# Optimization experiments

Measured on AMD Instinct MI355X. Metric: run time of the kernel, lower is better.

Reference implementation:

```python
import jax, jax.numpy as jnp
import numpy as np

K = 3
STRIDE = 1
PAD = 1
DIL = 1


def conv2d(x, w, b, stride, pad, dil):
    y = jax.lax.conv_general_dilated(
        x, w, (stride, stride), [(pad, pad), (pad, pad)],
        rhs_dilation=(dil, dil), dimension_numbers=("NCHW", "OIHW", "NCHW"))
    return y + b[None, :, None, None]


def bilinear_gather(img, ys, xs):
    # img: (C,H,W); ys,xs: (KK,Ho,Wo) pixel coords.
    # grid_sample(mode=bilinear, padding_mode=zeros, align_corners=True):
    # out-of-range corners contribute 0, interpolation weights unchanged.
    H, W = img.shape[-2:]
    y0 = jnp.floor(ys)
    x0 = jnp.floor(xs)
    wy1 = ys - y0
    wx1 = xs - x0
    wy0 = 1.0 - wy1
    wx0 = 1.0 - wx1

    def g(yc, xc):
        yi = yc.astype(jnp.int32)
        xi = xc.astype(jnp.int32)
        valid = (yi >= 0) & (yi < H) & (xi >= 0) & (xi < W)
        yi = jnp.clip(yi, 0, H - 1)
        xi = jnp.clip(xi, 0, W - 1)
        v = img[:, yi, xi]  # (C,KK,Ho,Wo)
        return v * valid[None].astype(img.dtype)

    return (g(y0, x0) * (wy0 * wx0)[None]
            + g(y0, x0 + 1.0) * (wy0 * wx1)[None]
            + g(y0 + 1.0, x0) * (wy1 * wx0)[None]
            + g(y0 + 1.0, x0 + 1.0) * (wy1 * wx1)[None])


def setup_inputs() -> dict:
    key = jax.random.key(0)
    ks = jax.random.split(key, 4)
    B, C_in, H, W = 8, 64, 96, 96
    C_out = 64
    x = jax.random.normal(ks[0], (B, C_in, H, W), dtype=jnp.float32)
    weight = jax.random.normal(ks[1], (C_out, C_in, K, K), dtype=jnp.float32) * 0.05
    bias = jax.random.normal(ks[2], (C_out,), dtype=jnp.float32) * 0.01
    off_w = jax.random.normal(ks[3], (2 * K * K, C_in, K, K), dtype=jnp.float32) * 0.05
    off_b = jnp.zeros((2 * K * K,), dtype=jnp.float32)
    return {"x": x, "weight": weight, "bias": bias, "off_w": off_w, "off_b": off_b}


def reference(x, weight, bias, off_w, off_b):
    B, C, H, W = x.shape
    Ho = (H + 2 * PAD - DIL * (K - 1) - 1) // STRIDE + 1
    Wo = (W + 2 * PAD - DIL * (K - 1) - 1) // STRIDE + 1

    offsets = conv2d(x, off_w, off_b, STRIDE, PAD, DIL)  # (B,2*K*K,Ho,Wo)
    off = offsets.reshape(B, K * K, 2, Ho, Wo)

    # Base sampling grid (note: original code does NOT subtract padding; kept faithful).
    by, bx = jnp.meshgrid(jnp.arange(Ho, dtype=x.dtype), jnp.arange(Wo, dtype=x.dtype), indexing="ij")
    by = by * STRIDE + (K // 2) * DIL
    bx = bx * STRIDE + (K // 2) * DIL
    ko = jnp.arange(-(K // 2), K // 2 + 1, dtype=x.dtype)
    ky, kx = jnp.meshgrid(ko, ko, indexing="ij")

    sy = by[None, None] + ky.reshape(1, -1, 1, 1) + off[:, :, 0]  # (B,KK,Ho,Wo)
    sx = bx[None, None] + kx.reshape(1, -1, 1, 1) + off[:, :, 1]

    sampled = jax.vmap(bilinear_gather)(x, sy, sx)  # (B,C,KK,Ho,Wo)

    wflat = weight.reshape(weight.shape[0], C, K * K)  # (O,C,KK)
    out = jnp.einsum("bckhw,ock->bohw", sampled, wflat)
    return out + bias[None, :, None, None]
```

## Files before the change

### kernel.cpp

```cpp
#include <hip/hip_runtime.h>

#define HH 96
#define WW 96
#define HW 9216
#define CIN 64
#define COUT 64
#define NB 8

typedef __bf16 bf16x8 __attribute__((ext_vector_type(8)));
typedef float  f32x4  __attribute__((ext_vector_type(4)));

__device__ __forceinline__ unsigned short f2bf_bits(float f) {
    unsigned u = __float_as_uint(f);
    unsigned r = u + 0x7FFFu + ((u >> 16) & 1u);
    return (unsigned short)(r >> 16);
}
__device__ __forceinline__ float bf2f(unsigned short s) {
    return __uint_as_float(((unsigned)s) << 16);
}

__global__ __launch_bounds__(256) void xcvt_prep(const float* __restrict__ x,
                                                 const float* __restrict__ weight,
                                                 const float* __restrict__ off_w,
                                                 unsigned short* __restrict__ xt,
                                                 unsigned short* __restrict__ wTb,
                                                 unsigned short* __restrict__ owTb) {
    int bid   = blockIdx.x;
    int t     = threadIdx.x;
    int b     = bid & 7;
    int pbase = (bid >> 3) * 64;
    int pl    = t & 63;
    int q     = t >> 6;
    int p     = pbase + pl;

    const float* xp = x + ((size_t)(b * 64 + q * 16)) * HW + p;
    unsigned short hbits[16];
#pragma unroll
    for (int i = 0; i < 16; ++i) hbits[i] = f2bf_bits(xp[(size_t)i * HW]);

    uint4 w0, w1;
    w0.x = hbits[0]  | (hbits[1]  << 16);
    w0.y = hbits[2]  | (hbits[3]  << 16);
    w0.z = hbits[4]  | (hbits[5]  << 16);
    w0.w = hbits[6]  | (hbits[7]  << 16);
    w1.x = hbits[8]  | (hbits[9]  << 16);
    w1.y = hbits[10] | (hbits[11] << 16);
    w1.z = hbits[12] | (hbits[13] << 16);
    w1.w = hbits[14] | (hbits[15] << 16);
    unsigned short* dst = xt + ((size_t)(b * HW + p)) * 64 + q * 16;
    *(uint4*)dst       = w0;
    *(uint4*)(dst + 8) = w1;

    if (bid < 216) {
        int i = bid * 256 + t;
        if (i < 36864) {
            int tap = i >> 12;
            int co  = (i >> 6) & 63;
            int c   = i & 63;
            wTb[i] = f2bf_bits(weight[(co * 64 + c) * 9 + tap]);
        } else {
            int f  = i - 36864;
            int j  = f / 576;
            int kk = f - j * 576;
            int tap = kk >> 6;
            int c   = kk & 63;
            owTb[f] = (j < 18) ? f2bf_bits(off_w[((j * 64 + c) * 9) + tap]) : (unsigned short)0;
        }
    }
}

__global__ __launch_bounds__(256, 4) void offs_mfma(const unsigned short* __restrict__ xt,
                                                    const unsigned short* __restrict__ owTb,
                                                    const float* __restrict__ ob,
                                                    float* __restrict__ off) {
    __shared__ unsigned short S[64 * 72];

    int bid   = blockIdx.x;
    int t     = threadIdx.x;
    int b     = bid & 7;
    int pbase = (bid >> 3) * 64;

    int pl = t & 63;
    int cg = t >> 6;
    int px = pbase + pl;
    int h  = px / WW;
    int w  = px - h * WW;

    int ln = t & 15;
    int qd = (t >> 4) & 3;
    int pt = t >> 6;

    f32x4 accj[2] = {{0.f, 0.f, 0.f, 0.f}, {0.f, 0.f, 0.f, 0.f}};

    const unsigned short* xb = xt + (size_t)b * HW * 64;

    for (int tap = 0; tap < 9; ++tap) {
        int r  = tap / 3, s = tap - r * 3;
        int iy = h - 1 + r, ix = w - 1 + s;
        bool valid = (iy >= 0) & (iy < HH) & (ix >= 0) & (ix < WW);
        uint4 va = {0u, 0u, 0u, 0u}, vb = {0u, 0u, 0u, 0u};
        if (valid) {
            const uint4* p = (const uint4*)(xb + ((size_t)(iy * WW + ix)) * 64 + cg * 16);
            va = p[0];
            vb = p[1];
        }
        *(uint4*)&S[pl * 72 + cg * 16]     = va;
        *(uint4*)&S[pl * 72 + cg * 16 + 8] = vb;
        __syncthreads();

        bf16x8 a0 = *(const bf16x8*)&S[(pt * 16 + ln) * 72 + qd * 8];
        bf16x8 a1 = *(const bf16x8*)&S[(pt * 16 + ln) * 72 + 32 + qd * 8];
#pragma unroll
        for (int jt = 0; jt < 2; ++jt) {
            const unsigned short* brow = owTb + (size_t)(jt * 16 + ln) * 576 + tap * 64 + qd * 8;
            bf16x8 b0 = *(const bf16x8*)brow;
            bf16x8 b1 = *(const bf16x8*)(brow + 32);
            accj[jt] = __builtin_amdgcn_mfma_f32_16x16x32_bf16(a0, b0, accj[jt], 0, 0, 0);
            accj[jt] = __builtin_amdgcn_mfma_f32_16x16x32_bf16(a1, b1, accj[jt], 0, 0, 0);
        }
        __syncthreads();
    }

    int pxo = pbase + pt * 16 + qd * 4;
    {
        float bv = ob[ln];
        float4 st;
        st.x = accj[0].x + bv; st.y = accj[0].y + bv;
        st.z = accj[0].z + bv; st.w = accj[0].w + bv;
        *(float4*)(off + ((size_t)(b * 18 + ln)) * HW + pxo) = st;
    }
    if (ln < 2) {
        int   j  = 16 + ln;
        float bv = ob[j];
        float4 st;
        st.x = accj[1].x + bv; st.y = accj[1].y + bv;
        st.z = accj[1].z + bv; st.w = accj[1].w + bv;
        *(float4*)(off + ((size_t)(b * 18 + j)) * HW + pxo) = st;
    }
}

__global__ __launch_bounds__(256, 4) void deform_main(const unsigned short* __restrict__ xt,
                                                      const unsigned short* __restrict__ wTb,
                                                      const float* __restrict__ bias,
                                                      const float* __restrict__ off,
                                                      float* __restrict__ out) {
    __shared__ unsigned short S[64 * 72];
    __shared__ unsigned short Wk[64 * 72];

    int bid   = blockIdx.x;
    int t     = threadIdx.x;
    int b     = bid & 7;
    int pbase = (bid >> 3) * 64;

    int pl = t & 63;
    int cg = t >> 6;
    int px = pbase + pl;
    int h  = px / WW;
    int w  = px - h * WW;

    int ln = t & 15;
    int qd = (t >> 4) & 3;
    int ct = t >> 6;

    const unsigned short* xb = xt + (size_t)b * HW * 64;
    const float* offb = off + (size_t)b * 18 * HW + px;

    float offy[9], offx[9];
#pragma unroll
    for (int k = 0; k < 9; ++k) {
        offy[k] = offb[(2 * k) * HW];
        offx[k] = offb[(2 * k + 1) * HW];
    }

    f32x4 acc[4] = {{0.f,0.f,0.f,0.f},{0.f,0.f,0.f,0.f},{0.f,0.f,0.f,0.f},{0.f,0.f,0.f,0.f}};

    for (int tap = 0; tap < 9; ++tap) {
        int   r = tap / 3, s = tap - r * 3;
        float sy = (float)(h + r) + offy[tap];
        float sx = (float)(w + s) + offx[tap];
        float fy = floorf(sy), fx = floorf(sx);
        int   y0 = (int)fy, x0 = (int)fx;
        int   y1 = y0 + 1, x1 = x0 + 1;
        float wy1 = sy - fy, wx1 = sx - fx;
        float wy0 = 1.f - wy1, wx0 = 1.f - wx1;

        float m00 = (y0 >= 0 && y0 < HH && x0 >= 0 && x0 < WW) ? 1.f : 0.f;
        float m01 = (y0 >= 0 && y0 < HH && x1 >= 0 && x1 < WW) ? 1.f : 0.f;
        float m10 = (y1 >= 0 && y1 < HH && x0 >= 0 && x0 < WW) ? 1.f : 0.f;
        float m11 = (y1 >= 0 && y1 < HH && x1 >= 0 && x1 < WW) ? 1.f : 0.f;

        int cy0 = min(max(y0, 0), HH - 1), cy1 = min(max(y1, 0), HH - 1);
        int cx0 = min(max(x0, 0), WW - 1), cx1 = min(max(x1, 0), WW - 1);
        float w00 = wy0 * wx0 * m00, w01 = wy0 * wx1 * m01;
        float w10 = wy1 * wx0 * m10, w11 = wy1 * wx1 * m11;

        const uint4* p00 = (const uint4*)(xb + ((size_t)(cy0 * WW + cx0)) * 64 + cg * 16);
        const uint4* p01 = (const uint4*)(xb + ((size_t)(cy0 * WW + cx1)) * 64 + cg * 16);
        const uint4* p10 = (const uint4*)(xb + ((size_t)(cy1 * WW + cx0)) * 64 + cg * 16);
        const uint4* p11 = (const uint4*)(xb + ((size_t)(cy1 * WW + cx1)) * 64 + cg * 16);
        uint4 c00[2] = {p00[0], p00[1]};
        uint4 c01[2] = {p01[0], p01[1]};
        uint4 c10[2] = {p10[0], p10[1]};
        uint4 c11[2] = {p11[0], p11[1]};

        unsigned short ov[16];
#pragma unroll
        for (int g = 0; g < 2; ++g) {
            const unsigned short* q00 = (const unsigned short*)&c00[g];
            const unsigned short* q01 = (const unsigned short*)&c01[g];
            const unsigned short* q10 = (const unsigned short*)&c10[g];
            const unsigned short* q11 = (const unsigned short*)&c11[g];
#pragma unroll
            for (int i = 0; i < 8; ++i) {
                float v = w00 * bf2f(q00[i]) + w01 * bf2f(q01[i])
                        + w10 * bf2f(q10[i]) + w11 * bf2f(q11[i]);
                ov[g * 8 + i] = f2bf_bits(v);
            }
        }
        uint4 s0, s1;
        s0.x = ov[0]  | (ov[1]  << 16); s0.y = ov[2]  | (ov[3]  << 16);
        s0.z = ov[4]  | (ov[5]  << 16); s0.w = ov[6]  | (ov[7]  << 16);
        s1.x = ov[8]  | (ov[9]  << 16); s1.y = ov[10] | (ov[11] << 16);
        s1.z = ov[12] | (ov[13] << 16); s1.w = ov[14] | (ov[15] << 16);
        *(uint4*)&S[pl * 72 + cg * 16]     = s0;
        *(uint4*)&S[pl * 72 + cg * 16 + 8] = s1;

        {
            const uint4* wsrc = (const uint4*)(wTb + (size_t)tap * 4096);
            uint4 a  = wsrc[2 * t];
            uint4 b2 = wsrc[2 * t + 1];
            int co = t >> 2, c0 = (t & 3) * 16;
            *(uint4*)&Wk[co * 72 + c0]     = a;
            *(uint4*)&Wk[co * 72 + c0 + 8] = b2;
        }
        __syncthreads();

        bf16x8 b0 = *(const bf16x8*)&Wk[(ct * 16 + ln) * 72 + qd * 8];
        bf16x8 b1 = *(const bf16x8*)&Wk[(ct * 16 + ln) * 72 + 32 + qd * 8];
#pragma unroll
        for (int pt = 0; pt < 4; ++pt) {
            bf16x8 a0 = *(const bf16x8*)&S[(pt * 16 + ln) * 72 + qd * 8];
            bf16x8 a1 = *(const bf16x8*)&S[(pt * 16 + ln) * 72 + 32 + qd * 8];
            acc[pt] = __builtin_amdgcn_mfma_f32_16x16x32_bf16(a0, b0, acc[pt], 0, 0, 0);
            acc[pt] = __builtin_amdgcn_mfma_f32_16x16x32_bf16(a1, b1, acc[pt], 0, 0, 0);
        }
        __syncthreads();
    }

    int   co = ct * 16 + ln;
    float bv = bias[co];
    float* ob2 = out + ((size_t)(b * 64 + co)) * HW + pbase + qd * 4;
#pragma unroll
    for (int pt = 0; pt < 4; ++pt) {
        float4 st;
        st.x = acc[pt].x + bv; st.y = acc[pt].y + bv;
        st.z = acc[pt].z + bv; st.w = acc[pt].w + bv;
        *(float4*)(ob2 + pt * 16) = st;
    }
}

extern "C" void kernel_launch(void* const* d_in, const int* in_sizes, int n_in,
                              void* d_out, int out_size, void* d_ws, size_t ws_size,
                              hipStream_t stream) {
    const float* x      = (const float*)d_in[0];
    const float* weight = (const float*)d_in[1];
    const float* bias   = (const float*)d_in[2];
    const float* off_w  = (const float*)d_in[3];
    const float* off_b  = (const float*)d_in[4];
    float* out = (float*)d_out;

    float*          offbuf = (float*)d_ws;
    unsigned short* xt     = (unsigned short*)(offbuf + 1327104);
    unsigned short* wTb    = xt + 4718592;
    unsigned short* owTb   = wTb + 36864;

    hipLaunchKernelGGL(xcvt_prep,   dim3(1152), dim3(256), 0, stream,
                       x, weight, off_w, xt, wTb, owTb);
    hipLaunchKernelGGL(offs_mfma,   dim3(1152), dim3(256), 0, stream,
                       xt, owTb, off_b, offbuf);
    hipLaunchKernelGGL(deform_main, dim3(1152), dim3(256), 0, stream,
                       xt, wTb, bias, offbuf, out);
}
```

Before: 161.7 us.

## Software-pipeline gather loads across taps and coalesce transposed bf16 stores

The deform and offset-conv kernels now issue the global loads for tap t+1 (bilinear corner gathers, weight tiles, B-fragments) into registers before processing tap t. This overlaps memory latency with the interpolation math and MFMA work. The prep kernel now transposes through shared memory so each block writes its NHWC bf16 tile contiguously. The launch-bounds occupancy hints are dropped, so register use will rise and occupancy may fall.

New measurement: 163.2 us. Within noise of the previous version (+0.9%).

```diff
diff --git a/kernel.cpp b/kernel.cpp
--- a/kernel.cpp
+++ b/kernel.cpp
@@ -3,12 +3,12 @@
 #define HH 96
 #define WW 96
 #define HW 9216
-#define CIN 64
-#define COUT 64
 #define NB 8
 
 typedef __bf16 bf16x8 __attribute__((ext_vector_type(8)));
 typedef float  f32x4  __attribute__((ext_vector_type(4)));
+
+union BF8 { uint4 u; bf16x8 v; unsigned short s[8]; };
 
 __device__ __forceinline__ unsigned short f2bf_bits(float f) {
     unsigned u = __float_as_uint(f);
@@ -25,31 +25,33 @@
                                                  unsigned short* __restrict__ xt,
                                                  unsigned short* __restrict__ wTb,
                                                  unsigned short* __restrict__ owTb) {
+    __shared__ unsigned short T[64 * 72];
     int bid   = blockIdx.x;
     int t     = threadIdx.x;
     int b     = bid & 7;
     int pbase = (bid >> 3) * 64;
     int pl    = t & 63;
     int q     = t >> 6;
-    int p     = pbase + pl;
-
-    const float* xp = x + ((size_t)(b * 64 + q * 16)) * HW + p;
-    unsigned short hbits[16];
-#pragma unroll
-    for (int i = 0; i < 16; ++i) hbits[i] = f2bf_bits(xp[(size_t)i * HW]);
+
+    const float* xp = x + ((size_t)(b * 64 + q * 16)) * HW + pbase + pl;
+    unsigned short hb[16];
+#pragma unroll
+    for (int i = 0; i < 16; ++i) hb[i] = f2bf_bits(xp[(size_t)i * HW]);
 
     uint4 w0, w1;
-    w0.x = hbits[0]  | (hbits[1]  << 16);
-    w0.y = hbits[2]  | (hbits[3]  << 16);
-    w0.z = hbits[4]  | (hbits[5]  << 16);
-    w0.w = hbits[6]  | (hbits[7]  << 16);
-    w1.x = hbits[8]  | (hbits[9]  << 16);
-    w1.y = hbits[10] | (hbits[11] << 16);
-    w1.z = hbits[12] | (hbits[13] << 16);
-    w1.w = hbits[14] | (hbits[15] << 16);
-    unsigned short* dst = xt + ((size_t)(b * HW + p)) * 64 + q * 16;
-    *(uint4*)dst       = w0;
-    *(uint4*)(dst + 8) = w1;
+    w0.x = hb[0]  | (hb[1]  << 16); w0.y = hb[2]  | (hb[3]  << 16);
+    w0.z = hb[4]  | (hb[5]  << 16); w0.w = hb[6]  | (hb[7]  << 16);
+    w1.x = hb[8]  | (hb[9]  << 16); w1.y = hb[10] | (hb[11] << 16);
+    w1.z = hb[12] | (hb[13] << 16); w1.w = hb[14] | (hb[15] << 16);
+    *(uint4*)&T[pl * 72 + q * 16]     = w0;
+    *(uint4*)&T[pl * 72 + q * 16 + 8] = w1;
+    __syncthreads();
+
+    uint4 a  = *(const uint4*)&T[(t >> 2) * 72 + (t & 3) * 16];
+    uint4 b2 = *(const uint4*)&T[(t >> 2) * 72 + (t & 3) * 16 + 8];
+    unsigned short* dst = xt + ((size_t)(b * HW + pbase)) * 64 + t * 16;
+    *(uint4*)dst       = a;
+    *(uint4*)(dst + 8) = b2;
 
     if (bid < 216) {
         int i = bid * 256 + t;
@@ -59,20 +61,20 @@
             int c   = i & 63;
             wTb[i] = f2bf_bits(weight[(co * 64 + c) * 9 + tap]);
         } else {
-            int f  = i - 36864;
-            int j  = f / 576;
-            int kk = f - j * 576;
+            int f   = i - 36864;
+            int j   = f / 576;
+            int kk  = f - j * 576;
             int tap = kk >> 6;
             int c   = kk & 63;
-            owTb[f] = (j < 18) ? f2bf_bits(off_w[((j * 64 + c) * 9) + tap]) : (unsigned short)0;
-        }
-    }
-}
-
-__global__ __launch_bounds__(256, 4) void offs_mfma(const unsigned short* __restrict__ xt,
-                                                    const unsigned short* __restrict__ owTb,
-                                                    const float* __restrict__ ob,
-                                                    float* __restrict__ off) {
+            owTb[f] = (j < 18) ? f2bf_bits(off_w[(j * 64 + c) * 9 + tap]) : (unsigned short)0;
+        }
+    }
+}
+
+__global__ __launch_bounds__(256) void offs_mfma(const unsigned short* __restrict__ xt,
+                                                 const unsigned short* __restrict__ owTb,
+                                                 const float* __restrict__ ob,
+                                                 float* __restrict__ off) {
     __shared__ unsigned short S[64 * 72];
 
     int bid   = blockIdx.x;
@@ -94,31 +96,54 @@
 
     const unsigned short* xb = xt + (size_t)b * HW * 64;
 
+    uint4 pa, pb, paN, pbN;
+    uint4 br00, br01, br10, br11, br00N, br01N, br10N, br11N;
+
+    {
+        int  iy = h - 1, ix = w - 1;
+        bool valid = (iy >= 0) & (ix >= 0);
+        int  cy = max(iy, 0), cx = max(ix, 0);
+        const uint4* p = (const uint4*)(xb + ((size_t)(cy * WW + cx)) * 64 + cg * 16);
+        pa = p[0]; pb = p[1];
+        if (!valid) { pa = make_uint4(0,0,0,0); pb = make_uint4(0,0,0,0); }
+        const unsigned short* b0p = owTb + (size_t)ln * 576 + qd * 8;
+        const unsigned short* b1p = owTb + (size_t)(16 + ln) * 576 + qd * 8;
+        br00 = *(const uint4*)b0p;  br01 = *(const uint4*)(b0p + 32);
+        br10 = *(const uint4*)b1p;  br11 = *(const uint4*)(b1p + 32);
+    }
+
     for (int tap = 0; tap < 9; ++tap) {
-        int r  = tap / 3, s = tap - r * 3;
-        int iy = h - 1 + r, ix = w - 1 + s;
-        bool valid = (iy >= 0) & (iy < HH) & (ix >= 0) & (ix < WW);
-        uint4 va = {0u, 0u, 0u, 0u}, vb = {0u, 0u, 0u, 0u};
-        if (valid) {
-            const uint4* p = (const uint4*)(xb + ((size_t)(iy * WW + ix)) * 64 + cg * 16);
-            va = p[0];
-            vb = p[1];
-        }
-        *(uint4*)&S[pl * 72 + cg * 16]     = va;
-        *(uint4*)&S[pl * 72 + cg * 16 + 8] = vb;
+        if (tap < 8) {
+            int  tn = tap + 1;
+            int  r  = tn / 3, s = tn - r * 3;
+            int  iy = h - 1 + r, ix = w - 1 + s;
+            bool valid = (iy >= 0) & (iy < HH) & (ix >= 0) & (ix < WW);
+            int  cy = min(max(iy, 0), HH - 1), cx = min(max(ix, 0), WW - 1);
+            const uint4* p = (const uint4*)(xb + ((size_t)(cy * WW + cx)) * 64 + cg * 16);
+            paN = p[0]; pbN = p[1];
+            if (!valid) { paN = make_uint4(0,0,0,0); pbN = make_uint4(0,0,0,0); }
+            const unsigned short* b0p = owTb + (size_t)ln * 576 + tn * 64 + qd * 8;
+            const unsigned short* b1p = owTb + (size_t)(16 + ln) * 576 + tn * 64 + qd * 8;
+            br00N = *(const uint4*)b0p;  br01N = *(const uint4*)(b0p + 32);
+            br10N = *(const uint4*)b1p;  br11N = *(const uint4*)(b1p + 32);
+        }
+
+        *(uint4*)&S[pl * 72 + cg * 16]     = pa;
+        *(uint4*)&S[pl * 72 + cg * 16 + 8] = pb;
         __syncthreads();
 
-        bf16x8 a0 = *(const bf16x8*)&S[(pt * 16 + ln) * 72 + qd * 8];
-        bf16x8 a1 = *(const bf16x8*)&S[(pt * 16 + ln) * 72 + 32 + qd * 8];
-#pragma unroll
-        for (int jt = 0; jt < 2; ++jt) {
-            const unsigned short* brow = owTb + (size_t)(jt * 16 + ln) * 576 + tap * 64 + qd * 8;
-            bf16x8 b0 = *(const bf16x8*)brow;
-            bf16x8 b1 = *(const bf16x8*)(brow + 32);
-            accj[jt] = __builtin_amdgcn_mfma_f32_16x16x32_bf16(a0, b0, accj[jt], 0, 0, 0);
-            accj[jt] = __builtin_amdgcn_mfma_f32_16x16x32_bf16(a1, b1, accj[jt], 0, 0, 0);
-        }
+        BF8 a0, a1, u00, u01, u10, u11;
+        a0.u = *(const uint4*)&S[(pt * 16 + ln) * 72 + qd * 8];
+        a1.u = *(const uint4*)&S[(pt * 16 + ln) * 72 + 32 + qd * 8];
+        u00.u = br00; u01.u = br01; u10.u = br10; u11.u = br11;
+        accj[0] = __builtin_amdgcn_mfma_f32_16x16x32_bf16(a0.v, u00.v, accj[0], 0, 0, 0);
+        accj[0] = __builtin_amdgcn_mfma_f32_16x16x32_bf16(a1.v, u01.v, accj[0], 0, 0, 0);
+        accj[1] = __builtin_amdgcn_mfma_f32_16x16x32_bf16(a0.v, u10.v, accj[1], 0, 0, 0);
+        accj[1] = __builtin_amdgcn_mfma_f32_16x16x32_bf16(a1.v, u11.v, accj[1], 0, 0, 0);
         __syncthreads();
+
+        pa = paN; pb = pbN;
+        br00 = br00N; br01 = br01N; br10 = br10N; br11 = br11N;
     }
 
     int pxo = pbase + pt * 16 + qd * 4;
@@ -139,11 +164,11 @@
     }
 }
 
-__global__ __launch_bounds__(256, 4) void deform_main(const unsigned short* __restrict__ xt,
-                                                      const unsigned short* __restrict__ wTb,
-                                                      const float* __restrict__ bias,
-                                                      const float* __restrict__ off,
-                                                      float* __restrict__ out) {
+__global__ __launch_bounds__(256) void deform_main(const unsigned short* __restrict__ xt,
+                                                   const unsigned short* __restrict__ wTb,
+                                                   const float* __restrict__ bias,
+                                                   const float* __restrict__ off,
+                                                   float* __restrict__ out) {
     __shared__ unsigned short S[64 * 72];
     __shared__ unsigned short Wk[64 * 72];
 
@@ -174,78 +199,97 @@
 
     f32x4 acc[4] = {{0.f,0.f,0.f,0.f},{0.f,0.f,0.f,0.f},{0.f,0.f,0.f,0.f},{0.f,0.f,0.f,0.f}};
 
+    uint4 c00a, c00b, c01a, c01b, c10a, c10b, c11a, c11b, wk0, wk1;
+    uint4 c00aN, c00bN, c01aN, c01bN, c10aN, c10bN, c11aN, c11bN, wk0N, wk1N;
+    float w00, w01, w10, w11, w00N, w01N, w10N, w11N;
+
+#define ISSUE_TAP(TAP, A00,B00,A01,B01,A10,B10,A11,B11, WA,WB, W0,W1,W2,W3)            \
+    {                                                                                   \
+        int   r = (TAP) / 3, s = (TAP) - r * 3;                                         \
+        float sy = (float)(h + r) + offy[(TAP)];                                        \
+        float sx = (float)(w + s) + offx[(TAP)];                                        \
+        float fy = floorf(sy), fx = floorf(sx);                                         \
+        int   y0 = (int)fy, x0 = (int)fx;                                               \
+        int   y1 = y0 + 1, x1 = x0 + 1;                                                 \
+        float wy1 = sy - fy, wx1 = sx - fx;                                             \
+        float wy0 = 1.f - wy1, wx0 = 1.f - wx1;                                         \
+        float m00 = (y0 >= 0 && y0 < HH && x0 >= 0 && x0 < WW) ? 1.f : 0.f;             \
+        float m01 = (y0 >= 0 && y0 < HH && x1 >= 0 && x1 < WW) ? 1.f : 0.f;             \
+        float m10 = (y1 >= 0 && y1 < HH && x0 >= 0 && x0 < WW) ? 1.f : 0.f;             \
+        float m11 = (y1 >= 0 && y1 < HH && x1 >= 0 && x1 < WW) ? 1.f : 0.f;             \
+        int cy0 = min(max(y0, 0), HH - 1), cy1 = min(max(y1, 0), HH - 1);               \
+        int cx0 = min(max(x0, 0), WW - 1), cx1 = min(max(x1, 0), WW - 1);               \
+        W0 = wy0 * wx0 * m00; W1 = wy0 * wx1 * m01;                                     \
+        W2 = wy1 * wx0 * m10; W3 = wy1 * wx1 * m11;                                     \
+        const uint4* p00 = (const uint4*)(xb + ((size_t)(cy0 * WW + cx0)) * 64 + cg * 16); \
+        const uint4* p01 = (const uint4*)(xb + ((size_t)(cy0 * WW + cx1)) * 64 + cg * 16); \
+        const uint4* p10 = (const uint4*)(xb + ((size_t)(cy1 * WW + cx0)) * 64 + cg * 16); \
+        const uint4* p11 = (const uint4*)(xb + ((size_t)(cy1 * WW + cx1)) * 64 + cg * 16); \
+        A00 = p00[0]; B00 = p00[1];                                                     \
+        A01 = p01[0]; B01 = p01[1];                                                     \
+        A10 = p10[0]; B10 = p10[1];                                                     \
+        A11 = p11[0]; B11 = p11[1];                                                     \
+        const uint4* wsrc = (const uint4*)(wTb + (size_t)(TAP) * 4096);                 \
+        WA = wsrc[2 * t]; WB = wsrc[2 * t + 1];                                         \
+    }
+
+    ISSUE_TAP(0, c00a,c00b,c01a,c01b,c10a,c10b,c11a,c11b, wk0,wk1, w00,w01,w10,w11);
+
     for (int tap = 0; tap < 9; ++tap) {
-        int   r = tap / 3, s = tap - r * 3;
-        float sy = (float)(h + r) + offy[tap];
-        float sx = (float)(w + s) + offx[tap];
-        float fy = floorf(sy), fx = floorf(sx);
-        int   y0 = (int)fy, x0 = (int)fx;
-        int   y1 = y0 + 1, x1 = x0 + 1;
-        float wy1 = sy - fy, wx1 = sx - fx;
-        float wy0 = 1.f - wy1, wx0 = 1.f - wx1;
-
-        float m00 = (y0 >= 0 && y0 < HH && x0 >= 0 && x0 < WW) ? 1.f : 0.f;
-        float m01 = (y0 >= 0 && y0 < HH && x1 >= 0 && x1 < WW) ? 1.f : 0.f;
-        float m10 = (y1 >= 0 && y1 < HH && x0 >= 0 && x0 < WW) ? 1.f : 0.f;
-        float m11 = (y1 >= 0 && y1 < HH && x1 >= 0 && x1 < WW) ? 1.f : 0.f;
-
-        int cy0 = min(max(y0, 0), HH - 1), cy1 = min(max(y1, 0), HH - 1);
-        int cx0 = min(max(x0, 0), WW - 1), cx1 = min(max(x1, 0), WW - 1);
-        float w00 = wy0 * wx0 * m00, w01 = wy0 * wx1 * m01;
-        float w10 = wy1 * wx0 * m10, w11 = wy1 * wx1 * m11;
-
-        const uint4* p00 = (const uint4*)(xb + ((size_t)(cy0 * WW + cx0)) * 64 + cg * 16);
-        const uint4* p01 = (const uint4*)(xb + ((size_t)(cy0 * WW + cx1)) * 64 + cg * 16);
-        const uint4* p10 = (const uint4*)(xb + ((size_t)(cy1 * WW + cx0)) * 64 + cg * 16);
-        const uint4* p11 = (const uint4*)(xb + ((size_t)(cy1 * WW + cx1)) * 64 + cg * 16);
-        uint4 c00[2] = {p00[0], p00[1]};
-        uint4 c01[2] = {p01[0], p01[1]};
-        uint4 c10[2] = {p10[0], p10[1]};
-        uint4 c11[2] = {p11[0], p11[1]};
-
-        unsigned short ov[16];
-#pragma unroll
-        for (int g = 0; g < 2; ++g) {
-            const unsigned short* q00 = (const unsigned short*)&c00[g];
-            const unsigned short* q01 = (const unsigned short*)&c01[g];
-            const unsigned short* q10 = (const unsigned short*)&c10[g];
-            const unsigned short* q11 = (const unsigned short*)&c11[g];
+        if (tap < 8) {
+            ISSUE_TAP(tap + 1, c00aN,c00bN,c01aN,c01bN,c10aN,c10bN,c11aN,c11bN,
+                      wk0N,wk1N, w00N,w01N,w10N,w11N);
+        }
+
+        {
+            BF8 q00a, q00b, q01a, q01b, q10a, q10b, q11a, q11b;
+            q00a.u = c00a; q00b.u = c00b; q01a.u = c01a; q01b.u = c01b;
+            q10a.u = c10a; q10b.u = c10b; q11a.u = c11a; q11b.u = c11b;
+            unsigned short ov[16];
 #pragma unroll
             for (int i = 0; i < 8; ++i) {
-                float v = w00 * bf2f(q00[i]) + w01 * bf2f(q01[i])
-                        + w10 * bf2f(q10[i]) + w11 * bf2f(q11[i]);
-                ov[g * 8 + i] = f2bf_bits(v);
+                float v0 = w00 * bf2f(q00a.s[i]) + w01 * bf2f(q01a.s[i])
+                         + w10 * bf2f(q10a.s[i]) + w11 * bf2f(q11a.s[i]);
+                float v1 = w00 * bf2f(q00b.s[i]) + w01 * bf2f(q01b.s[i])
+                         + w10 * bf2f(q10b.s[i]) + w11 * bf2f(q11b.s[i]);
+                ov[i]     = f2bf_bits(v0);
+                ov[8 + i] = f2bf_bits(v1);
             }
-        }
-        uint4 s0, s1;
-        s0.x = ov[0]  | (ov[1]  << 16); s0.y = ov[2]  | (ov[3]  << 16);
-        s0.z = ov[4]  | (ov[5]  << 16); s0.w = ov[6]  | (ov[7]  << 16);
-        s1.x = ov[8]  | (ov[9]  << 16); s1.y = ov[10] | (ov[11] << 16);
-        s1.z = ov[12] | (ov[13] << 16); s1.w = ov[14] | (ov[15] << 16);
-        *(uint4*)&S[pl * 72 + cg * 16]     = s0;
-        *(uint4*)&S[pl * 72 + cg * 16 + 8] = s1;
+            uint4 s0, s1;
+            s0.x = ov[0]  | (ov[1]  << 16); s0.y = ov[2]  | (ov[3]  << 16);
+            s0.z = ov[4]  | (ov[5]  << 16); s0.w = ov[6]  | (ov[7]  << 16);
+            s1.x = ov[8]  | (ov[9]  << 16); s1.y = ov[10] | (ov[11] << 16);
+            s1.z = ov[12] | (ov[13] << 16); s1.w = ov[14] | (ov[15] << 16);
+            *(uint4*)&S[pl * 72 + cg * 16]     = s0;
+            *(uint4*)&S[pl * 72 + cg * 16 + 8] = s1;
+
+            int co = t >> 2, c0 = (t & 3) * 16;
+            *(uint4*)&Wk[co * 72 + c0]     = wk0;
+            *(uint4*)&Wk[co * 72 + c0 + 8] = wk1;
+        }
+        __syncthreads();
 
         {
-            const uint4* wsrc = (const uint4*)(wTb + (size_t)tap * 4096);
-            uint4 a  = wsrc[2 * t];
-            uint4 b2 = wsrc[2 * t + 1];
-            int co = t >> 2, c0 = (t & 3) * 16;
-            *(uint4*)&Wk[co * 72 + c0]     = a;
-            *(uint4*)&Wk[co * 72 + c0 + 8] = b2;
+            BF8 b0, b1;
+            b0.u = *(const uint4*)&Wk[(ct * 16 + ln) * 72 + qd * 8];
+            b1.u = *(const uint4*)&Wk[(ct * 16 + ln) * 72 + 32 + qd * 8];
+#pragma unroll
+            for (int pt = 0; pt < 4; ++pt) {
+                BF8 a0, a1;
+                a0.u = *(const uint4*)&S[(pt * 16 + ln) * 72 + qd * 8];
+                a1.u = *(const uint4*)&S[(pt * 16 + ln) * 72 + 32 + qd * 8];
+                acc[pt] = __builtin_amdgcn_mfma_f32_16x16x32_bf16(a0.v, b0.v, acc[pt], 0, 0, 0);
+                acc[pt] = __builtin_amdgcn_mfma_f32_16x16x32_bf16(a1.v, b1.v, acc[pt], 0, 0, 0);
+            }
         }
         __syncthreads();
 
-        bf16x8 b0 = *(const bf16x8*)&Wk[(ct * 16 + ln) * 72 + qd * 8];
-        bf16x8 b1 = *(const bf16x8*)&Wk[(ct * 16 + ln) * 72 + 32 + qd * 8];
-#pragma unroll
-        for (int pt = 0; pt < 4; ++pt) {
-            bf16x8 a0 = *(const bf16x8*)&S[(pt * 16 + ln) * 72 + qd * 8];
-            bf16x8 a1 = *(const bf16x8*)&S[(pt * 16 + ln) * 72 + 32 + qd * 8];
-            acc[pt] = __builtin_amdgcn_mfma_f32_16x16x32_bf16(a0, b0, acc[pt], 0, 0, 0);
-            acc[pt] = __builtin_amdgcn_mfma_f32_16x16x32_bf16(a1, b1, acc[pt], 0, 0, 0);
-        }
-        __syncthreads();
-    }
+        c00a = c00aN; c00b = c00bN; c01a = c01aN; c01b = c01bN;
+        c10a = c10aN; c10b = c10bN; c11a = c11aN; c11b = c11bN;
+        wk0 = wk0N; wk1 = wk1N;
+        w00 = w00N; w01 = w01N; w10 = w10N; w11 = w11N;
+    }
+#undef ISSUE_TAP
 
     int   co = ct * 16 + ln;
     float bv = bias[co];
```

## Coalesce pixel-major gathers, XOR-swizzle LDS tiles, and prefetch offsets per tap

Applied to the files above, without the earlier changes.

The gather work is remapped so that 8 consecutive threads each read 16 bytes of one pixel's 64-channel row, giving coalesced 128-byte reads, and each thread handles two pixels. The LDS tiles drop the 72-element padding in favour of an XOR swizzle on 16-byte chunks to avoid bank conflicts. The transpose in xcvt_prep is staged through shared memory so its global writes become contiguous. In deform_main the offsets for the next tap are loaded during the current tap instead of all 18 values up front, and the occupancy hint in launch_bounds is removed.

Measured after the change: 136.4 us. 15.7% less time.

```diff
diff --git a/kernel.cpp b/kernel.cpp
--- a/kernel.cpp
+++ b/kernel.cpp
@@ -3,12 +3,12 @@
 #define HH 96
 #define WW 96
 #define HW 9216
-#define CIN 64
-#define COUT 64
 #define NB 8
 
 typedef __bf16 bf16x8 __attribute__((ext_vector_type(8)));
 typedef float  f32x4  __attribute__((ext_vector_type(4)));
+
+union BF8 { uint4 u; bf16x8 v; unsigned short s[8]; };
 
 __device__ __forceinline__ unsigned short f2bf_bits(float f) {
     unsigned u = __float_as_uint(f);
@@ -17,6 +17,27 @@
 }
 __device__ __forceinline__ float bf2f(unsigned short s) {
     return __uint_as_float(((unsigned)s) << 16);
+}
+
+__device__ __forceinline__ void bl_setup(int h, int w, int r, int s, float oy, float ox,
+                                         int* a, float* wg) {
+    float sy = (float)(h + r) + oy;
+    float sx = (float)(w + s) + ox;
+    float fy = floorf(sy), fx = floorf(sx);
+    int   y0 = (int)fy, x0 = (int)fx;
+    int   y1 = y0 + 1, x1 = x0 + 1;
+    float wy1 = sy - fy, wx1 = sx - fx;
+    float wy0 = 1.f - wy1, wx0 = 1.f - wx1;
+    float m00 = (y0 >= 0 && y0 < HH && x0 >= 0 && x0 < WW) ? 1.f : 0.f;
+    float m01 = (y0 >= 0 && y0 < HH && x1 >= 0 && x1 < WW) ? 1.f : 0.f;
+    float m10 = (y1 >= 0 && y1 < HH && x0 >= 0 && x0 < WW) ? 1.f : 0.f;
+    float m11 = (y1 >= 0 && y1 < HH && x1 >= 0 && x1 < WW) ? 1.f : 0.f;
+    int cy0 = min(max(y0, 0), HH - 1), cy1 = min(max(y1, 0), HH - 1);
+    int cx0 = min(max(x0, 0), WW - 1), cx1 = min(max(x1, 0), WW - 1);
+    a[0] = (cy0 * WW + cx0) * 64;  a[1] = (cy0 * WW + cx1) * 64;
+    a[2] = (cy1 * WW + cx0) * 64;  a[3] = (cy1 * WW + cx1) * 64;
+    wg[0] = wy0 * wx0 * m00;  wg[1] = wy0 * wx1 * m01;
+    wg[2] = wy1 * wx0 * m10;  wg[3] = wy1 * wx1 * m11;
 }
 
 __global__ __launch_bounds__(256) void xcvt_prep(const float* __restrict__ x,
@@ -25,31 +46,35 @@
                                                  unsigned short* __restrict__ xt,
                                                  unsigned short* __restrict__ wTb,
                                                  unsigned short* __restrict__ owTb) {
+    __shared__ unsigned short T[64 * 64];
     int bid   = blockIdx.x;
     int t     = threadIdx.x;
     int b     = bid & 7;
     int pbase = (bid >> 3) * 64;
     int pl    = t & 63;
     int q     = t >> 6;
-    int p     = pbase + pl;
-
-    const float* xp = x + ((size_t)(b * 64 + q * 16)) * HW + p;
-    unsigned short hbits[16];
-#pragma unroll
-    for (int i = 0; i < 16; ++i) hbits[i] = f2bf_bits(xp[(size_t)i * HW]);
+
+    const float* xp = x + ((size_t)(b * 64 + q * 16)) * HW + pbase + pl;
+    unsigned short hb[16];
+#pragma unroll
+    for (int i = 0; i < 16; ++i) hb[i] = f2bf_bits(xp[(size_t)i * HW]);
 
     uint4 w0, w1;
-    w0.x = hbits[0]  | (hbits[1]  << 16);
-    w0.y = hbits[2]  | (hbits[3]  << 16);
-    w0.z = hbits[4]  | (hbits[5]  << 16);
-    w0.w = hbits[6]  | (hbits[7]  << 16);
-    w1.x = hbits[8]  | (hbits[9]  << 16);
-    w1.y = hbits[10] | (hbits[11] << 16);
-    w1.z = hbits[12] | (hbits[13] << 16);
-    w1.w = hbits[14] | (hbits[15] << 16);
-    unsigned short* dst = xt + ((size_t)(b * HW + p)) * 64 + q * 16;
-    *(uint4*)dst       = w0;
-    *(uint4*)(dst + 8) = w1;
+    w0.x = hb[0]  | (hb[1]  << 16); w0.y = hb[2]  | (hb[3]  << 16);
+    w0.z = hb[4]  | (hb[5]  << 16); w0.w = hb[6]  | (hb[7]  << 16);
+    w1.x = hb[8]  | (hb[9]  << 16); w1.y = hb[10] | (hb[11] << 16);
+    w1.z = hb[12] | (hb[13] << 16); w1.w = hb[14] | (hb[15] << 16);
+    int sw = pl & 7;
+    *(uint4*)&T[pl * 64 + (((2 * q)     ^ sw) << 3)] = w0;
+    *(uint4*)&T[pl * 64 + (((2 * q + 1) ^ sw) << 3)] = w1;
+    __syncthreads();
+
+    int row = t >> 2, rs = row & 7;
+    uint4 a  = *(const uint4*)&T[row * 64 + ((((t & 3) * 2)     ^ rs) << 3)];
+    uint4 b2 = *(const uint4*)&T[row * 64 + ((((t & 3) * 2 + 1) ^ rs) << 3)];
+    unsigned short* dst = xt + ((size_t)(b * HW + pbase)) * 64 + t * 16;
+    *(uint4*)dst       = a;
+    *(uint4*)(dst + 8) = b2;
 
     if (bid < 216) {
         int i = bid * 256 + t;
@@ -59,64 +84,72 @@
             int c   = i & 63;
             wTb[i] = f2bf_bits(weight[(co * 64 + c) * 9 + tap]);
         } else {
-            int f  = i - 36864;
-            int j  = f / 576;
-            int kk = f - j * 576;
+            int f   = i - 36864;
+            int j   = f / 576;
+            int kk  = f - j * 576;
             int tap = kk >> 6;
             int c   = kk & 63;
-            owTb[f] = (j < 18) ? f2bf_bits(off_w[((j * 64 + c) * 9) + tap]) : (unsigned short)0;
-        }
-    }
-}
-
-__global__ __launch_bounds__(256, 4) void offs_mfma(const unsigned short* __restrict__ xt,
-                                                    const unsigned short* __restrict__ owTb,
-                                                    const float* __restrict__ ob,
-                                                    float* __restrict__ off) {
-    __shared__ unsigned short S[64 * 72];
+            owTb[f] = (j < 18) ? f2bf_bits(off_w[(j * 64 + c) * 9 + tap]) : (unsigned short)0;
+        }
+    }
+}
+
+__global__ __launch_bounds__(256) void offs_mfma(const unsigned short* __restrict__ xt,
+                                                 const unsigned short* __restrict__ owTb,
+                                                 const float* __restrict__ ob,
+                                                 float* __restrict__ off) {
+    __shared__ unsigned short S[64 * 64];
 
     int bid   = blockIdx.x;
     int t     = threadIdx.x;
     int b     = bid & 7;
     int pbase = (bid >> 3) * 64;
 
-    int pl = t & 63;
-    int cg = t >> 6;
-    int px = pbase + pl;
-    int h  = px / WW;
-    int w  = px - h * WW;
+    int e    = t & 7;
+    int base = t >> 3;
+    int px0  = pbase + base;
+    int px1  = px0 + 32;
+    int h0 = px0 / WW, w0 = px0 - h0 * WW;
+    int h1 = px1 / WW, w1 = px1 - h1 * WW;
+    int sw = base & 7;
 
     int ln = t & 15;
     int qd = (t >> 4) & 3;
     int pt = t >> 6;
 
     f32x4 accj[2] = {{0.f, 0.f, 0.f, 0.f}, {0.f, 0.f, 0.f, 0.f}};
-
     const unsigned short* xb = xt + (size_t)b * HW * 64;
 
     for (int tap = 0; tap < 9; ++tap) {
-        int r  = tap / 3, s = tap - r * 3;
-        int iy = h - 1 + r, ix = w - 1 + s;
-        bool valid = (iy >= 0) & (iy < HH) & (ix >= 0) & (ix < WW);
-        uint4 va = {0u, 0u, 0u, 0u}, vb = {0u, 0u, 0u, 0u};
-        if (valid) {
-            const uint4* p = (const uint4*)(xb + ((size_t)(iy * WW + ix)) * 64 + cg * 16);
-            va = p[0];
-            vb = p[1];
-        }
-        *(uint4*)&S[pl * 72 + cg * 16]     = va;
-        *(uint4*)&S[pl * 72 + cg * 16 + 8] = vb;
+        int r = tap / 3, s = tap - r * 3;
+
+        int  iy0 = h0 - 1 + r, ix0 = w0 - 1 + s;
+        bool v0  = (iy0 >= 0) & (iy0 < HH) & (ix0 >= 0) & (ix0 < WW);
+        int  a0  = (min(max(iy0, 0), HH - 1) * WW + min(max(ix0, 0), WW - 1)) * 64;
+        int  iy1 = h1 - 1 + r, ix1 = w1 - 1 + s;
+        bool v1  = (iy1 >= 0) & (iy1 < HH) & (ix1 >= 0) & (ix1 < WW);
+        int  a1  = (min(max(iy1, 0), HH - 1) * WW + min(max(ix1, 0), WW - 1)) * 64;
+
+        uint4 p0 = *(const uint4*)(xb + a0 + e * 8);
+        uint4 p1 = *(const uint4*)(xb + a1 + e * 8);
+        if (!v0) p0 = make_uint4(0, 0, 0, 0);
+        if (!v1) p1 = make_uint4(0, 0, 0, 0);
+        *(uint4*)&S[base * 64 + ((e ^ sw) << 3)]        = p0;
+        *(uint4*)&S[(base + 32) * 64 + ((e ^ sw) << 3)] = p1;
         __syncthreads();
 
-        bf16x8 a0 = *(const bf16x8*)&S[(pt * 16 + ln) * 72 + qd * 8];
-        bf16x8 a1 = *(const bf16x8*)&S[(pt * 16 + ln) * 72 + 32 + qd * 8];
+        int  row = pt * 16 + ln, rs = row & 7;
+        BF8  fa0, fa1;
+        fa0.u = *(const uint4*)&S[row * 64 + ((qd       ^ rs) << 3)];
+        fa1.u = *(const uint4*)&S[row * 64 + (((qd + 4) ^ rs) << 3)];
 #pragma unroll
         for (int jt = 0; jt < 2; ++jt) {
             const unsigned short* brow = owTb + (size_t)(jt * 16 + ln) * 576 + tap * 64 + qd * 8;
-            bf16x8 b0 = *(const bf16x8*)brow;
-            bf16x8 b1 = *(const bf16x8*)(brow + 32);
-            accj[jt] = __builtin_amdgcn_mfma_f32_16x16x32_bf16(a0, b0, accj[jt], 0, 0, 0);
-            accj[jt] = __builtin_amdgcn_mfma_f32_16x16x32_bf16(a1, b1, accj[jt], 0, 0, 0);
+            BF8 fb0, fb1;
+            fb0.u = *(const uint4*)brow;
+            fb1.u = *(const uint4*)(brow + 32);
+            accj[jt] = __builtin_amdgcn_mfma_f32_16x16x32_bf16(fa0.v, fb0.v, accj[jt], 0, 0, 0);
+            accj[jt] = __builtin_amdgcn_mfma_f32_16x16x32_bf16(fa1.v, fb1.v, accj[jt], 0, 0, 0);
         }
         __syncthreads();
     }
@@ -139,112 +172,119 @@
     }
 }
 
-__global__ __launch_bounds__(256, 4) void deform_main(const unsigned short* __restrict__ xt,
-                                                      const unsigned short* __restrict__ wTb,
-                                                      const float* __restrict__ bias,
-                                                      const float* __restrict__ off,
-                                                      float* __restrict__ out) {
-    __shared__ unsigned short S[64 * 72];
-    __shared__ unsigned short Wk[64 * 72];
+__global__ __launch_bounds__(256) void deform_main(const unsigned short* __restrict__ xt,
+                                                   const unsigned short* __restrict__ wTb,
+                                                   const float* __restrict__ bias,
+                                                   const float* __restrict__ off,
+                                                   float* __restrict__ out) {
+    __shared__ unsigned short S[64 * 64];
+    __shared__ unsigned short Wk[64 * 64];
 
     int bid   = blockIdx.x;
     int t     = threadIdx.x;
     int b     = bid & 7;
     int pbase = (bid >> 3) * 64;
 
-    int pl = t & 63;
-    int cg = t >> 6;
-    int px = pbase + pl;
-    int h  = px / WW;
-    int w  = px - h * WW;
+    int e    = t & 7;
+    int base = t >> 3;
+    int px0  = pbase + base;
+    int px1  = px0 + 32;
+    int h0 = px0 / WW, w0 = px0 - h0 * WW;
+    int h1 = px1 / WW, w1 = px1 - h1 * WW;
+    int sw = base & 7;
 
     int ln = t & 15;
     int qd = (t >> 4) & 3;
     int ct = t >> 6;
 
     const unsigned short* xb = xt + (size_t)b * HW * 64;
-    const float* offb = off + (size_t)b * 18 * HW + px;
-
-    float offy[9], offx[9];
-#pragma unroll
-    for (int k = 0; k < 9; ++k) {
-        offy[k] = offb[(2 * k) * HW];
-        offx[k] = offb[(2 * k + 1) * HW];
-    }
+    const float* offb = off + (size_t)b * 18 * HW;
 
     f32x4 acc[4] = {{0.f,0.f,0.f,0.f},{0.f,0.f,0.f,0.f},{0.f,0.f,0.f,0.f},{0.f,0.f,0.f,0.f}};
 
+    float oy0 = offb[0 * HW + px0], ox0 = offb[1 * HW + px0];
+    float oy1 = offb[0 * HW + px1], ox1 = offb[1 * HW + px1];
+
     for (int tap = 0; tap < 9; ++tap) {
-        int   r = tap / 3, s = tap - r * 3;
-        float sy = (float)(h + r) + offy[tap];
-        float sx = (float)(w + s) + offx[tap];
-        float fy = floorf(sy), fx = floorf(sx);
-        int   y0 = (int)fy, x0 = (int)fx;
-        int   y1 = y0 + 1, x1 = x0 + 1;
-        float wy1 = sy - fy, wx1 = sx - fx;
-        float wy0 = 1.f - wy1, wx0 = 1.f - wx1;
-
-        float m00 = (y0 >= 0 && y0 < HH && x0 >= 0 && x0 < WW) ? 1.f : 0.f;
-        float m01 = (y0 >= 0 && y0 < HH && x1 >= 0 && x1 < WW) ? 1.f : 0.f;
-        float m10 = (y1 >= 0 && y1 < HH && x0 >= 0 && x0 < WW) ? 1.f : 0.f;
-        float m11 = (y1 >= 0 && y1 < HH && x1 >= 0 && x1 < WW) ? 1.f : 0.f;
-
-        int cy0 = min(max(y0, 0), HH - 1), cy1 = min(max(y1, 0), HH - 1);
-        int cx0 = min(max(x0, 0), WW - 1), cx1 = min(max(x1, 0), WW - 1);
-        float w00 = wy0 * wx0 * m00, w01 = wy0 * wx1 * m01;
-        float w10 = wy1 * wx0 * m10, w11 = wy1 * wx1 * m11;
-
-        const uint4* p00 = (const uint4*)(xb + ((size_t)(cy0 * WW + cx0)) * 64 + cg * 16);
-        const uint4* p01 = (const uint4*)(xb + ((size_t)(cy0 * WW + cx1)) * 64 + cg * 16);
-        const uint4* p10 = (const uint4*)(xb + ((size_t)(cy1 * WW + cx0)) * 64 + cg * 16);
-        const uint4* p11 = (const uint4*)(xb + ((size_t)(cy1 * WW + cx1)) * 64 + cg * 16);
-        uint4 c00[2] = {p00[0], p00[1]};
-        uint4 c01[2] = {p01[0], p01[1]};
-        uint4 c10[2] = {p10[0], p10[1]};
-        uint4 c11[2] = {p11[0], p11[1]};
-
-        unsigned short ov[16];
-#pragma unroll
-        for (int g = 0; g < 2; ++g) {
-            const unsigned short* q00 = (const unsigned short*)&c00[g];
-            const unsigned short* q01 = (const unsigned short*)&c01[g];
-            const unsigned short* q10 = (const unsigned short*)&c10[g];
-            const unsigned short* q11 = (const unsigned short*)&c11[g];
-#pragma unroll
-            for (int i = 0; i < 8; ++i) {
-                float v = w00 * bf2f(q00[i]) + w01 * bf2f(q01[i])
-                        + w10 * bf2f(q10[i]) + w11 * bf2f(q11[i]);
-                ov[g * 8 + i] = f2bf_bits(v);
-            }
-        }
-        uint4 s0, s1;
-        s0.x = ov[0]  | (ov[1]  << 16); s0.y = ov[2]  | (ov[3]  << 16);
-        s0.z = ov[4]  | (ov[5]  << 16); s0.w = ov[6]  | (ov[7]  << 16);
-        s1.x = ov[8]  | (ov[9]  << 16); s1.y = ov[10] | (ov[11] << 16);
-        s1.z = ov[12] | (ov[13] << 16); s1.w = ov[14] | (ov[15] << 16);
-        *(uint4*)&S[pl * 72 + cg * 16]     = s0;
-        *(uint4*)&S[pl * 72 + cg * 16 + 8] = s1;
+        int r = tap / 3, s = tap - r * 3;
+
+        int   a0[4], a1[4];
+        float g0[4], g1[4];
+        bl_setup(h0, w0, r, s, oy0, ox0, a0, g0);
+        bl_setup(h1, w1, r, s, oy1, ox1, a1, g1);
+
+        uint4 cA[4], cB[4];
+#pragma unroll
+        for (int c = 0; c < 4; ++c) cA[c] = *(const uint4*)(xb + a0[c] + e * 8);
+#pragma unroll
+        for (int c = 0; c < 4; ++c) cB[c] = *(const uint4*)(xb + a1[c] + e * 8);
+
+        float oy0N = 0.f, ox0N = 0.f, oy1N = 0.f, ox1N = 0.f;
+        if (tap < 8) {
+            oy0N = offb[(2 * tap + 2) * HW + px0]; ox0N = offb[(2 * tap + 3) * HW + px0];
+            oy1N = offb[(2 * tap + 2) * HW + px1]; ox1N = offb[(2 * tap + 3) * HW + px1];
+        }
 
         {
             const uint4* wsrc = (const uint4*)(wTb + (size_t)tap * 4096);
-            uint4 a  = wsrc[2 * t];
-            uint4 b2 = wsrc[2 * t + 1];
-            int co = t >> 2, c0 = (t & 3) * 16;
-            *(uint4*)&Wk[co * 72 + c0]     = a;
-            *(uint4*)&Wk[co * 72 + c0 + 8] = b2;
+            uint4 wa = wsrc[2 * t];
+            uint4 wb = wsrc[2 * t + 1];
+            int co = t >> 2, cs = co & 7;
+            int c0 = (t & 3) * 2;
+            *(uint4*)&Wk[co * 64 + ((c0       ^ cs) << 3)] = wa;
+            *(uint4*)&Wk[co * 64 + (((c0 + 1) ^ cs) << 3)] = wb;
+        }
+
+        {
+            BF8 q0, q1, q2, q3;
+            q0.u = cA[0]; q1.u = cA[1]; q2.u = cA[2]; q3.u = cA[3];
+            unsigned short ov[8];
+#pragma unroll
+            for (int i = 0; i < 8; ++i) {
+                float v = g0[0] * bf2f(q0.s[i]) + g0[1] * bf2f(q1.s[i])
+                        + g0[2] * bf2f(q2.s[i]) + g0[3] * bf2f(q3.s[i]);
+                ov[i] = f2bf_bits(v);
+            }
+            uint4 sv;
+            sv.x = ov[0] | (ov[1] << 16); sv.y = ov[2] | (ov[3] << 16);
+            sv.z = ov[4] | (ov[5] << 16); sv.w = ov[6] | (ov[7] << 16);
+            *(uint4*)&S[base * 64 + ((e ^ sw) << 3)] = sv;
+        }
+        {
+            BF8 q0, q1, q2, q3;
+            q0.u = cB[0]; q1.u = cB[1]; q2.u = cB[2]; q3.u = cB[3];
+            unsigned short ov[8];
+#pragma unroll
+            for (int i = 0; i < 8; ++i) {
+                float v = g1[0] * bf2f(q0.s[i]) + g1[1] * bf2f(q1.s[i])
+                        + g1[2] * bf2f(q2.s[i]) + g1[3] * bf2f(q3.s[i]);
+                ov[i] = f2bf_bits(v);
+            }
+            uint4 sv;
+            sv.x = ov[0] | (ov[1] << 16); sv.y = ov[2] | (ov[3] << 16);
+            sv.z = ov[4] | (ov[5] << 16); sv.w = ov[6] | (ov[7] << 16);
+            *(uint4*)&S[(base + 32) * 64 + ((e ^ sw) << 3)] = sv;
         }
         __syncthreads();
 
-        bf16x8 b0 = *(const bf16x8*)&Wk[(ct * 16 + ln) * 72 + qd * 8];
-        bf16x8 b1 = *(const bf16x8*)&Wk[(ct * 16 + ln) * 72 + 32 + qd * 8];
-#pragma unroll
-        for (int pt = 0; pt < 4; ++pt) {
-            bf16x8 a0 = *(const bf16x8*)&S[(pt * 16 + ln) * 72 + qd * 8];
-            bf16x8 a1 = *(const bf16x8*)&S[(pt * 16 + ln) * 72 + 32 + qd * 8];
-            acc[pt] = __builtin_amdgcn_mfma_f32_16x16x32_bf16(a0, b0, acc[pt], 0, 0, 0);
-            acc[pt] = __builtin_amdgcn_mfma_f32_16x16x32_bf16(a1, b1, acc[pt], 0, 0, 0);
+        {
+            int  wrow = ct * 16 + ln, ws2 = wrow & 7;
+            BF8  fb0, fb1;
+            fb0.u = *(const uint4*)&Wk[wrow * 64 + ((qd       ^ ws2) << 3)];
+            fb1.u = *(const uint4*)&Wk[wrow * 64 + (((qd + 4) ^ ws2) << 3)];
+#pragma unroll
+            for (int pt = 0; pt < 4; ++pt) {
+                int row = pt * 16 + ln, rs = row & 7;
+                BF8 fa0, fa1;
+                fa0.u = *(const uint4*)&S[row * 64 + ((qd       ^ rs) << 3)];
+                fa1.u = *(const uint4*)&S[row * 64 + (((qd + 4) ^ rs) << 3)];
+                acc[pt] = __builtin_amdgcn_mfma_f32_16x16x32_bf16(fa0.v, fb0.v, acc[pt], 0, 0, 0);
+                acc[pt] = __builtin_amdgcn_mfma_f32_16x16x32_bf16(fa1.v, fb1.v, acc[pt], 0, 0, 0);
+            }
         }
         __syncthreads();
+
+        oy0 = oy0N; ox0 = ox0N; oy1 = oy1N; ox1 = ox1N;
     }
 
     int   co = ct * 16 + ln;
```
